# Kernel optimization log

Hardware: AMD Instinct MI355X
Metric: run time of the kernel (lower is better)

## Reference

```python
import jax, jax.numpy as jnp
import numpy as np

N_NODES = 50000
N_EDGES = 800000
FEAT = 10
HID = 64
N_SHEETS = 256
SHEET_LEN = 128
NUM_GRAPHS = 1


def _glorot(key, shape):
    fan_in, fan_out = shape[0], shape[1]
    lim = float(np.sqrt(6.0 / (fan_in + fan_out)))
    return jax.random.uniform(key, shape, jnp.float32, -lim, lim)


def setup_inputs() -> dict:
    key = jax.random.key(0)
    ks = jax.random.split(key, 16)
    x = jax.random.normal(ks[0], (N_NODES, FEAT), jnp.float32)
    edge_index = jax.random.randint(ks[1], (2, N_EDGES), 0, N_NODES, jnp.int64)
    batch = jnp.zeros((N_NODES,), jnp.int64)
    sheet_node_idx = jax.random.randint(ks[2], (N_SHEETS, SHEET_LEN), 0, N_NODES, jnp.int64)
    sheet_features = jax.random.normal(ks[3], (N_SHEETS, FEAT), jnp.float32)
    return {
        "x": x, "edge_index": edge_index, "batch": batch,
        "sheet_node_idx": sheet_node_idx, "sheet_features": sheet_features,
        "W_gcn1": _glorot(ks[4], (FEAT, HID)), "b_gcn1": jnp.zeros((HID,), jnp.float32),
        "W_gcn2": _glorot(ks[5], (HID, HID)), "b_gcn2": jnp.zeros((HID,), jnp.float32),
        "W_gcn3": _glorot(ks[6], (HID, HID)), "b_gcn3": jnp.zeros((HID,), jnp.float32),
        "geo_W1": _glorot(ks[7], (FEAT, HID)), "geo_b1": jnp.zeros((HID,), jnp.float32),
        "geo_W2": _glorot(ks[8], (HID, HID)), "geo_b2": jnp.zeros((HID,), jnp.float32),
        "fus_W": _glorot(ks[9], (2 * HID, HID)), "fus_b": jnp.zeros((HID,), jnp.float32),
        "q_W1": _glorot(ks[10], (2 * HID, HID)), "q_b1": jnp.zeros((HID,), jnp.float32),
        "q_W2": _glorot(ks[11], (HID, 1)), "q_b2": jnp.zeros((1,), jnp.float32),
    }


def gcn_conv(x, W, b, src, dst, norm_edge, norm_self):
    # PyG GCNConv: h = x @ W, symmetric-normalized aggregation with self loops, + b
    h = x @ W                                  # [N, H]
    msg = h[src] * norm_edge[:, None]          # [E, H] gather
    agg = jax.ops.segment_sum(msg, dst, num_segments=x.shape[0])  # scatter-add
    agg = agg + h * norm_self[:, None]         # self-loop contribution
    return agg + b


def reference(x, edge_index, batch, sheet_node_idx, sheet_features,
              W_gcn1, b_gcn1, W_gcn2, b_gcn2, W_gcn3, b_gcn3,
              geo_W1, geo_b1, geo_W2, geo_b2, fus_W, fus_b,
              q_W1, q_b1, q_W2, q_b2):
    src, dst = edge_index[0], edge_index[1]
    N = x.shape[0]
    # degree with self loops (edge weights = 1), counted on destination
    deg = jax.ops.segment_sum(jnp.ones_like(dst, jnp.float32), dst, num_segments=N) + 1.0
    dinv = jax.lax.rsqrt(deg)
    norm_edge = dinv[src] * dinv[dst]   # [E]
    norm_self = dinv * dinv             # [N]

    h = jax.nn.relu(gcn_conv(x, W_gcn1, b_gcn1, src, dst, norm_edge, norm_self))
    h = jax.nn.relu(gcn_conv(h, W_gcn2, b_gcn2, src, dst, norm_edge, norm_self))
    h = jax.nn.relu(gcn_conv(h, W_gcn3, b_gcn3, src, dst, norm_edge, norm_self))

    # global mean pool over batch ids (single graph here)
    sums = jax.ops.segment_sum(h, batch, num_segments=NUM_GRAPHS)
    counts = jax.ops.segment_sum(jnp.ones((N,), jnp.float32), batch, num_segments=NUM_GRAPHS)
    g_emb = sums / counts[:, None]      # [1, H]

    # per-sheet mean pooling (equal-length sheets)
    sheet_embs = h[sheet_node_idx].mean(axis=1)            # [S, H]

    geo = jax.nn.relu(sheet_features @ geo_W1 + geo_b1) @ geo_W2 + geo_b2
    fused = jax.nn.relu(jnp.concatenate([sheet_embs, geo], axis=1) @ fus_W + fus_b)

    global_embs = jnp.broadcast_to(g_emb, (fused.shape[0], g_emb.shape[1]))
    hq = jnp.concatenate([fused, global_embs], axis=1)
    q = jax.nn.relu(hq @ q_W1 + q_b1) @ q_W2 + q_b2
    return q[:, 0]
```

## Files before the change

kernel.cpp:

```cpp
#include <hip/hip_runtime.h>

#define HID 64
#define FEAT 10
#define MAXSEG 8192

typedef unsigned short u16;

__device__ __forceinline__ u16 f2bf(float f) {
    unsigned u = __float_as_uint(f);
    unsigned r = (u + 0x7fffu + ((u >> 16) & 1u)) >> 16;
    return (u16)r;
}
__device__ __forceinline__ void bf8_add(float* acc, uint4 u) {
    acc[0] += __uint_as_float(u.x << 16);
    acc[1] += __uint_as_float(u.x & 0xffff0000u);
    acc[2] += __uint_as_float(u.y << 16);
    acc[3] += __uint_as_float(u.y & 0xffff0000u);
    acc[4] += __uint_as_float(u.z << 16);
    acc[5] += __uint_as_float(u.z & 0xffff0000u);
    acc[6] += __uint_as_float(u.w << 16);
    acc[7] += __uint_as_float(u.w & 0xffff0000u);
}


__global__ void bin_kernel(const int* __restrict__ src, const int* __restrict__ dst,
                           int* __restrict__ gcnt, unsigned* __restrict__ tmp,
                           u16* __restrict__ hwb, u16* __restrict__ xp,
                           int E, int N) {
    __shared__ int h[256];
    int t = threadIdx.x, c = blockIdx.x;
    if (t < 256) h[t] = 0;
    __syncthreads();
    int b0 = c * 4096;
    unsigned pk[4]; int bk[4];
    #pragma unroll
    for (int j = 0; j < 4; j++) {
        int e = b0 + t + j * 1024;
        if (e < E) {
            int s = src[e], d = dst[e];
            pk[j] = ((unsigned)(d & 255) << 16) | (unsigned)s;
            bk[j] = d >> 8;
            atomicAdd(&h[bk[j]], 1);
        } else bk[j] = -1;
    }
    __syncthreads();
    if (t < 256) {
        int v = h[t];
        int resv = v ? atomicAdd(&gcnt[t], v) : 0;
        h[t] = t * MAXSEG + resv;
    }
    __syncthreads();
    #pragma unroll
    for (int j = 0; j < 4; j++) {
        if (bk[j] >= 0) {
            int slot = atomicAdd(&h[bk[j]], 1);
            tmp[slot] = pk[j];
        }
    }
    if (c == 0) {
        if (t < 64)      hwb[(size_t)N * 64 + t] = 0;
        else if (t < 80) xp[(size_t)N * 16 + (t - 64)] = 0;
    }
}

__global__ void csr_build(const unsigned* __restrict__ tmp, const int* __restrict__ gcnt,
                          u16* __restrict__ csr2,
                          int* __restrict__ row_start, int* __restrict__ row_cntp,
                          float* __restrict__ dinv,
                          const float* __restrict__ x, u16* __restrict__ xp, int N) {
    __shared__ __align__(16) u16 staged[MAXSEG];
    __shared__ int cntL[256], padL[256], scanL[256], curL[256];
    __shared__ float sdinv[256];
    int b = blockIdx.x, t = threadIdx.x;
    if (t < 256) cntL[t] = 0;
    for (int i = t; i < MAXSEG; i += 1024) staged[i] = (u16)N;
    __syncthreads();
    int segBase = b * MAXSEG, segLen = gcnt[b];
    for (int i = t; i < segLen; i += 1024)
        atomicAdd(&cntL[tmp[segBase + i] >> 16], 1);
    __syncthreads();
    if (t < 256) { padL[t] = (cntL[t] + 7) & ~7; scanL[t] = padL[t]; }
    __syncthreads();
    for (int off = 1; off < 256; off <<= 1) {
        int a = (t < 256) ? scanL[t] : 0;
        int s = (t >= off && t < 256) ? scanL[t - off] : 0;
        __syncthreads();
        if (t < 256) scanL[t] = a + s;
        __syncthreads();
    }
    if (t < 256) {
        int excl = scanL[t] - padL[t];
        curL[t] = excl;
        float dv = rsqrtf((float)cntL[t] + 1.0f);
        sdinv[t] = dv;
        int node = b * 256 + t;
        if (node < N) {
            row_start[node] = b * MAXSEG + excl;
            row_cntp[node]  = padL[t];
            dinv[node]      = dv;
        }
    }
    __syncthreads();
    for (int i = t; i < segLen; i += 1024) {
        unsigned e = tmp[segBase + i];
        int idx = atomicAdd(&curL[e >> 16], 1);
        staged[idx] = (u16)(e & 0xffffu);
    }
    for (int i = t; i < 256 * 16; i += 1024) {
        int nlc = i >> 4, cch = i & 15;
        int node = b * 256 + nlc;
        if (node < N)
            xp[(size_t)node * 16 + cch] =
                (cch < FEAT) ? f2bf(sdinv[nlc] * x[(size_t)node * FEAT + cch]) : (u16)0;
    }
    __syncthreads();
    ((uint4*)(csr2 + (size_t)b * MAXSEG))[t] = ((const uint4*)staged)[t];
}


__global__ void gxmm1(const int* __restrict__ row_start, const int* __restrict__ row_cntp,
                      const u16* __restrict__ csr2, const u16* __restrict__ xp,
                      const float* __restrict__ dinv,
                      const float* __restrict__ W1, const float* __restrict__ b1,
                      float* __restrict__ hf, int N) {
    __shared__ float sW[FEAT * 64];
    __shared__ float sH[64 * 16];
    int t = threadIdx.x;
    int node0 = blockIdx.x * 64;
    for (int i = t; i < FEAT * 64; i += 256) sW[i] = W1[i];
    if (t < 128) {
        int nl = t >> 1;
        int node = node0 + nl;
        int c0 = (t & 1) * 8;
        float acc[8] = {0.f,0.f,0.f,0.f,0.f,0.f,0.f,0.f};
        if (node < N) {
            uint4 sv = *(const uint4*)(xp + (size_t)node * 16 + c0);
            bf8_add(acc, sv);
            int i0 = row_start[node], iE = i0 + row_cntp[node];
            for (int i = i0; i < iE; i += 8) {
                uint4 ev = *(const uint4*)(csr2 + i);
                int s0 = ev.x & 0xffff, s1 = ev.x >> 16;
                int s2 = ev.y & 0xffff, s3 = ev.y >> 16;
                int s4 = ev.z & 0xffff, s5 = ev.z >> 16;
                int s6 = ev.w & 0xffff, s7 = ev.w >> 16;
                uint4 u0 = *(const uint4*)(xp + (size_t)s0 * 16 + c0);
                uint4 u1 = *(const uint4*)(xp + (size_t)s1 * 16 + c0);
                uint4 u2 = *(const uint4*)(xp + (size_t)s2 * 16 + c0);
                uint4 u3 = *(const uint4*)(xp + (size_t)s3 * 16 + c0);
                uint4 u4 = *(const uint4*)(xp + (size_t)s4 * 16 + c0);
                uint4 u5 = *(const uint4*)(xp + (size_t)s5 * 16 + c0);
                uint4 u6 = *(const uint4*)(xp + (size_t)s6 * 16 + c0);
                uint4 u7 = *(const uint4*)(xp + (size_t)s7 * 16 + c0);
                bf8_add(acc, u0); bf8_add(acc, u1); bf8_add(acc, u2); bf8_add(acc, u3);
                bf8_add(acc, u4); bf8_add(acc, u5); bf8_add(acc, u6); bf8_add(acc, u7);
            }
            float di = dinv[node];
            #pragma unroll
            for (int j = 0; j < 8; j++) acc[j] *= di;
        }
        #pragma unroll
        for (int j = 0; j < 8; j++) sH[nl * 16 + c0 + j] = acc[j];
    }
    __syncthreads();
    int c0 = (t & 15) * 4;
    int rbase = (t >> 4) * 4;
    float4 a0 = {0,0,0,0}, a1 = {0,0,0,0}, a2 = {0,0,0,0}, a3 = {0,0,0,0};
    for (int k = 0; k < FEAT; k++) {
        float4 w = *(const float4*)(sW + k * 64 + c0);
        float h0 = sH[(rbase + 0) * 16 + k];
        float h1v = sH[(rbase + 1) * 16 + k];
        float h2 = sH[(rbase + 2) * 16 + k];
        float h3 = sH[(rbase + 3) * 16 + k];
        a0.x += h0 * w.x; a0.y += h0 * w.y; a0.z += h0 * w.z; a0.w += h0 * w.w;
        a1.x += h1v * w.x; a1.y += h1v * w.y; a1.z += h1v * w.z; a1.w += h1v * w.w;
        a2.x += h2 * w.x; a2.y += h2 * w.y; a2.z += h2 * w.z; a2.w += h2 * w.w;
        a3.x += h3 * w.x; a3.y += h3 * w.y; a3.z += h3 * w.z; a3.w += h3 * w.w;
    }
    float4 bb = *(const float4*)(b1 + c0);
    float4 accs[4] = {a0, a1, a2, a3};
    for (int rr = 0; rr < 4; rr++) {
        int node = node0 + rbase + rr;
        if (node >= N) break;
        float4 v = accs[rr];
        v.x = fmaxf(v.x + bb.x, 0.f); v.y = fmaxf(v.y + bb.y, 0.f);
        v.z = fmaxf(v.z + bb.z, 0.f); v.w = fmaxf(v.w + bb.w, 0.f);
        *(float4*)(hf + (size_t)node * 64 + c0) = v;
    }
}


__global__ void gcn_matmul64(const float* __restrict__ h_in, const float* __restrict__ W,
                             const float* __restrict__ dinv, u16* __restrict__ hwb, int N) {
    __shared__ float sW[64 * 64];
    __shared__ float sH[64 * 65];
    int t = threadIdx.x;
    int node0 = blockIdx.x * 64;
    for (int i = t * 4; i < 4096; i += 1024)
        *(float4*)(sW + i) = *(const float4*)(W + i);
    for (int i = t; i < 4096; i += 256) {
        int r = i >> 6, k = i & 63;
        int node = node0 + r;
        sH[r * 65 + k] = (node < N) ? h_in[(size_t)node * 64 + k] : 0.0f;
    }
    __syncthreads();
    int c0 = (t & 15) * 4;
    int rbase = (t >> 4) * 4;
    float4 a0 = {0,0,0,0}, a1 = {0,0,0,0}, a2 = {0,0,0,0}, a3 = {0,0,0,0};
    for (int k = 0; k < 64; k++) {
        float4 w = *(const float4*)(sW + k * 64 + c0);
        float h0 = sH[(rbase + 0) * 65 + k];
        float h1v = sH[(rbase + 1) * 65 + k];
        float h2 = sH[(rbase + 2) * 65 + k];
        float h3 = sH[(rbase + 3) * 65 + k];
        a0.x += h0 * w.x; a0.y += h0 * w.y; a0.z += h0 * w.z; a0.w += h0 * w.w;
        a1.x += h1v * w.x; a1.y += h1v * w.y; a1.z += h1v * w.z; a1.w += h1v * w.w;
        a2.x += h2 * w.x; a2.y += h2 * w.y; a2.z += h2 * w.z; a2.w += h2 * w.w;
        a3.x += h3 * w.x; a3.y += h3 * w.y; a3.z += h3 * w.z; a3.w += h3 * w.w;
    }
    float4 accs[4] = {a0, a1, a2, a3};
    for (int rr = 0; rr < 4; rr++) {
        int node = node0 + rbase + rr;
        if (node >= N) break;
        float di = dinv[node];
        float4 v = accs[rr];
        ushort4 o;
        o.x = f2bf(v.x * di); o.y = f2bf(v.y * di);
        o.z = f2bf(v.z * di); o.w = f2bf(v.w * di);
        *(ushort4*)(hwb + (size_t)node * 64 + c0) = o;
    }
}

__global__ void gather_bf(const int* __restrict__ row_start, const int* __restrict__ row_cntp,
                          const u16* __restrict__ csr2, const u16* __restrict__ hwb,
                          const float* __restrict__ dinv, const float* __restrict__ b,
                          float* __restrict__ out, float* __restrict__ gsum,
                          int N, int do_gsum) {
    int t = threadIdx.x;
    int nl = t >> 3;
    int node = blockIdx.x * 32 + nl;
    int c0 = (t & 7) * 8;
    float acc[8] = {0.f,0.f,0.f,0.f,0.f,0.f,0.f,0.f};
    if (node < N) {
        uint4 sv = *(const uint4*)(hwb + (size_t)node * 64 + c0);
        bf8_add(acc, sv);
        int i0 = row_start[node], iE = i0 + row_cntp[node];
        for (int i = i0; i < iE; i += 8) {
            uint4 ev = *(const uint4*)(csr2 + i);
            int s0 = ev.x & 0xffff, s1 = ev.x >> 16;
            int s2 = ev.y & 0xffff, s3 = ev.y >> 16;
            int s4 = ev.z & 0xffff, s5 = ev.z >> 16;
            int s6 = ev.w & 0xffff, s7 = ev.w >> 16;
            uint4 u0 = *(const uint4*)(hwb + (size_t)s0 * 64 + c0);
            uint4 u1 = *(const uint4*)(hwb + (size_t)s1 * 64 + c0);
            uint4 u2 = *(const uint4*)(hwb + (size_t)s2 * 64 + c0);
            uint4 u3 = *(const uint4*)(hwb + (size_t)s3 * 64 + c0);
            uint4 u4 = *(const uint4*)(hwb + (size_t)s4 * 64 + c0);
            uint4 u5 = *(const uint4*)(hwb + (size_t)s5 * 64 + c0);
            uint4 u6 = *(const uint4*)(hwb + (size_t)s6 * 64 + c0);
            uint4 u7 = *(const uint4*)(hwb + (size_t)s7 * 64 + c0);
            bf8_add(acc, u0); bf8_add(acc, u1); bf8_add(acc, u2); bf8_add(acc, u3);
            bf8_add(acc, u4); bf8_add(acc, u5); bf8_add(acc, u6); bf8_add(acc, u7);
        }
        float di = dinv[node];
        const float4 bb0 = *(const float4*)(b + c0);
        const float4 bb1 = *(const float4*)(b + c0 + 4);
        float4 o0, o1;
        o0.x = fmaxf(acc[0]*di + bb0.x, 0.f); o0.y = fmaxf(acc[1]*di + bb0.y, 0.f);
        o0.z = fmaxf(acc[2]*di + bb0.z, 0.f); o0.w = fmaxf(acc[3]*di + bb0.w, 0.f);
        o1.x = fmaxf(acc[4]*di + bb1.x, 0.f); o1.y = fmaxf(acc[5]*di + bb1.y, 0.f);
        o1.z = fmaxf(acc[6]*di + bb1.z, 0.f); o1.w = fmaxf(acc[7]*di + bb1.w, 0.f);
        *(float4*)(out + (size_t)node * 64 + c0)     = o0;
        *(float4*)(out + (size_t)node * 64 + c0 + 4) = o1;
        acc[0]=o0.x; acc[1]=o0.y; acc[2]=o0.z; acc[3]=o0.w;
        acc[4]=o1.x; acc[5]=o1.y; acc[6]=o1.z; acc[7]=o1.w;
    }
    if (do_gsum) {
        __shared__ float red[32 * 64];
        #pragma unroll
        for (int j = 0; j < 8; j++) red[nl * 64 + c0 + j] = acc[j];
        __syncthreads();
        if (t < 64) {
            float s = 0.f;
            #pragma unroll 8
            for (int k = 0; k < 32; k++) s += red[k * 64 + t];
            atomicAdd(&gsum[t], s);
        }
    }
}


__global__ void final_kernel(const float* __restrict__ h3, const int* __restrict__ sheet_idx,
                             const float* __restrict__ sheet_feat, const float* __restrict__ g_sum,
                             const float* __restrict__ gW1, const float* __restrict__ gb1,
                             const float* __restrict__ gW2, const float* __restrict__ gb2,
                             const float* __restrict__ fW,  const float* __restrict__ fb,
                             const float* __restrict__ qW1, const float* __restrict__ qb1,
                             const float* __restrict__ qW2, const float* __restrict__ qb2,
                             float* __restrict__ out, int N, int L) {
    int s = blockIdx.x, t = threadIdx.x;
    __shared__ float red[256];
    __shared__ float semb[64];
    __shared__ float geoh[64];
    __shared__ float geo[64];
    __shared__ float hq[128];
    int c = t & 63, jg = t >> 6;
    float acc = 0.0f;
    for (int j = jg; j < L; j += 4) {
        int node = sheet_idx[s * L + j];
        acc += h3[(size_t)node * 64 + c];
    }
    red[t] = acc;
    __syncthreads();
    if (t < 64) {
        semb[t] = (red[t] + red[t + 64] + red[t + 128] + red[t + 192]) / (float)L;
        hq[64 + t] = g_sum[t] / (float)N;
        float a = gb1[t];
        #pragma unroll
        for (int k = 0; k < FEAT; k++) a += sheet_feat[s * FEAT + k] * gW1[k * 64 + t];
        geoh[t] = fmaxf(a, 0.0f);
    }
    __syncthreads();
    if (t < 64) {
        float a = gb2[t];
        for (int k = 0; k < 64; k++) a += geoh[k] * gW2[k * 64 + t];
        geo[t] = a;
    }
    __syncthreads();
    if (t < 64) {
        float a = fb[t];
        for (int k = 0; k < 64; k++) a += semb[k] * fW[k * 64 + t];
        for (int k = 0; k < 64; k++) a += geo[k]  * fW[(64 + k) * 64 + t];
        hq[t] = fmaxf(a, 0.0f);
    }
    __syncthreads();
    float q = 0.0f;
    if (t < 64) {
        float a = qb1[t];
        for (int k = 0; k < 128; k++) a += hq[k] * qW1[k * 64 + t];
        a = fmaxf(a, 0.0f);
        q = a * qW2[t];
        for (int off = 32; off > 0; off >>= 1) q += __shfl_down(q, off, 64);
        if (t == 0) out[s] = q + qb2[0];
    }
}

extern "C" void kernel_launch(void* const* d_in, const int* in_sizes, int n_in,
                              void* d_out, int out_size, void* d_ws, size_t ws_size,
                              hipStream_t stream) {
    const float* x          = (const float*)d_in[0];
    const int*   edge       = (const int*)d_in[1];
    const int*   sheet_idx  = (const int*)d_in[3];
    const float* sheet_feat = (const float*)d_in[4];
    const float* W1 = (const float*)d_in[5];  const float* b1 = (const float*)d_in[6];
    const float* W2 = (const float*)d_in[7];  const float* b2 = (const float*)d_in[8];
    const float* W3 = (const float*)d_in[9];  const float* b3 = (const float*)d_in[10];
    const float* gW1 = (const float*)d_in[11]; const float* gb1 = (const float*)d_in[12];
    const float* gW2 = (const float*)d_in[13]; const float* gb2 = (const float*)d_in[14];
    const float* fW  = (const float*)d_in[15]; const float* fb  = (const float*)d_in[16];
    const float* qW1 = (const float*)d_in[17]; const float* qb1 = (const float*)d_in[18];
    const float* qW2 = (const float*)d_in[19]; const float* qb2 = (const float*)d_in[20];
    float* out = (float*)d_out;

    int N = in_sizes[2];
    int E = in_sizes[1] / 2;
    int S = in_sizes[4] / FEAT;
    int L = in_sizes[3] / S;

    int nbuckets = (N + 255) / 256;
    int nchunks  = (E + 4095) / 4096;

    char* p = (char*)d_ws;
    unsigned* tmp  = (unsigned*)p;             p += (size_t)nbuckets * MAXSEG * 4;
    u16* csr2      = (u16*)p;                  p += (size_t)nbuckets * MAXSEG * 2;
    float* hf      = (float*)p;                p += (size_t)N * 64 * 4;
    u16* hwb       = (u16*)p;                  p += (size_t)(N + 1) * 64 * 2;
    u16* xp        = (u16*)p;                  p += (size_t)(N + 1) * 16 * 2;
    int* row_start = (int*)p;                  p += (size_t)N * 4;
    int* row_cntp  = (int*)p;                  p += (size_t)N * 4;
    float* dinv    = (float*)p;                p += (size_t)N * 4;
    int* gcnt      = (int*)p;                  p += 256 * 4;
    float* gsum    = (float*)p;                p += 64 * 4;

    hipMemsetAsync(gcnt, 0, 256 * 4 + 64 * 4, stream);

    const int* src = edge;
    const int* dst = edge + E;

    int gMM = (N + 63) / 64;
    int gGB = (N + 31) / 32;

    bin_kernel<<<nchunks, 1024, 0, stream>>>(src, dst, gcnt, tmp, hwb, xp, E, N);
    csr_build<<<nbuckets, 1024, 0, stream>>>(tmp, gcnt, csr2, row_start, row_cntp, dinv, x, xp, N);

    gxmm1<<<gMM, 256, 0, stream>>>(row_start, row_cntp, csr2, xp, dinv, W1, b1, hf, N);

    gcn_matmul64<<<gMM, 256, 0, stream>>>(hf, W2, dinv, hwb, N);
    gather_bf<<<gGB, 256, 0, stream>>>(row_start, row_cntp, csr2, hwb, dinv, b2, hf, gsum, N, 0);

    gcn_matmul64<<<gMM, 256, 0, stream>>>(hf, W3, dinv, hwb, N);
    gather_bf<<<gGB, 256, 0, stream>>>(row_start, row_cntp, csr2, hwb, dinv, b3, hf, gsum, N, 1);

    final_kernel<<<S, 256, 0, stream>>>(hf, sheet_idx, sheet_feat, gsum,
                                        gW1, gb1, gW2, gb2, fW, fb,
                                        qW1, qb1, qW2, qb2, out, N, L);
}
```

Before: 238.3 us.

## Sort nodes by degree within buckets to balance gather warps; prefetch CSR indices

csr_build now produces a per-bucket permutation that orders nodes by padded degree class, and the gather kernels (gxmm1, gather_bf) process nodes in that permuted order so threads in a wavefront have similar trip counts. The gather loops also prefetch the next 8-index CSR vector one iteration ahead, which needs a small pad at the end of csr2. The aim is to cut wavefront divergence and load latency in the neighbour aggregation, at the cost of an extra shared histogram and scan in csr_build, an indirect perm load per node, and scattered output writes.

```diff
diff --git a/kernel.cpp b/kernel.cpp
--- a/kernel.cpp
+++ b/kernel.cpp
@@ -66,13 +66,15 @@
 __global__ void csr_build(const unsigned* __restrict__ tmp, const int* __restrict__ gcnt,
                           u16* __restrict__ csr2,
                           int* __restrict__ row_start, int* __restrict__ row_cntp,
-                          float* __restrict__ dinv,
+                          float* __restrict__ dinv, int* __restrict__ perm,
                           const float* __restrict__ x, u16* __restrict__ xp, int N) {
     __shared__ __align__(16) u16 staged[MAXSEG];
     __shared__ int cntL[256], padL[256], scanL[256], curL[256];
     __shared__ float sdinv[256];
+    __shared__ int h32[32], o32[32];
     int b = blockIdx.x, t = threadIdx.x;
     if (t < 256) cntL[t] = 0;
+    if (t < 32) h32[t] = 0;
     for (int i = t; i < MAXSEG; i += 1024) staged[i] = (u16)N;
     __syncthreads();
     int segBase = b * MAXSEG, segLen = gcnt[b];
@@ -88,6 +90,7 @@
         if (t < 256) scanL[t] = a + s;
         __syncthreads();
     }
+    int key = 0;
     if (t < 256) {
         int excl = scanL[t] - padL[t];
         curL[t] = excl;
@@ -99,6 +102,18 @@
             row_cntp[node]  = padL[t];
             dinv[node]      = dv;
         }
+        key = min(padL[t] >> 3, 31);
+        atomicAdd(&h32[key], 1);
+    }
+    __syncthreads();
+    if (t == 0) {
+        int run = 0;
+        for (int k2 = 0; k2 < 32; k2++) { o32[k2] = run; run += h32[k2]; }
+    }
+    __syncthreads();
+    if (t < 256) {
+        int pos = atomicAdd(&o32[key], 1);
+        perm[b * 256 + pos] = b * 256 + t;
     }
     __syncthreads();
     for (int i = t; i < segLen; i += 1024) {
@@ -118,7 +133,8 @@
 }
 
 
-__global__ void gxmm1(const int* __restrict__ row_start, const int* __restrict__ row_cntp,
+__global__ void gxmm1(const int* __restrict__ perm,
+                      const int* __restrict__ row_start, const int* __restrict__ row_cntp,
                       const u16* __restrict__ csr2, const u16* __restrict__ xp,
                       const float* __restrict__ dinv,
                       const float* __restrict__ W1, const float* __restrict__ b1,
@@ -126,33 +142,38 @@
     __shared__ float sW[FEAT * 64];
     __shared__ float sH[64 * 16];
     int t = threadIdx.x;
-    int node0 = blockIdx.x * 64;
+    int slot0 = blockIdx.x * 64;
     for (int i = t; i < FEAT * 64; i += 256) sW[i] = W1[i];
     if (t < 128) {
         int nl = t >> 1;
-        int node = node0 + nl;
+        int node = perm[slot0 + nl];
         int c0 = (t & 1) * 8;
         float acc[8] = {0.f,0.f,0.f,0.f,0.f,0.f,0.f,0.f};
         if (node < N) {
             uint4 sv = *(const uint4*)(xp + (size_t)node * 16 + c0);
             bf8_add(acc, sv);
-            int i0 = row_start[node], iE = i0 + row_cntp[node];
-            for (int i = i0; i < iE; i += 8) {
-                uint4 ev = *(const uint4*)(csr2 + i);
-                int s0 = ev.x & 0xffff, s1 = ev.x >> 16;
-                int s2 = ev.y & 0xffff, s3 = ev.y >> 16;
-                int s4 = ev.z & 0xffff, s5 = ev.z >> 16;
-                int s6 = ev.w & 0xffff, s7 = ev.w >> 16;
-                uint4 u0 = *(const uint4*)(xp + (size_t)s0 * 16 + c0);
-                uint4 u1 = *(const uint4*)(xp + (size_t)s1 * 16 + c0);
-                uint4 u2 = *(const uint4*)(xp + (size_t)s2 * 16 + c0);
-                uint4 u3 = *(const uint4*)(xp + (size_t)s3 * 16 + c0);
-                uint4 u4 = *(const uint4*)(xp + (size_t)s4 * 16 + c0);
-                uint4 u5 = *(const uint4*)(xp + (size_t)s5 * 16 + c0);
-                uint4 u6 = *(const uint4*)(xp + (size_t)s6 * 16 + c0);
-                uint4 u7 = *(const uint4*)(xp + (size_t)s7 * 16 + c0);
-                bf8_add(acc, u0); bf8_add(acc, u1); bf8_add(acc, u2); bf8_add(acc, u3);
-                bf8_add(acc, u4); bf8_add(acc, u5); bf8_add(acc, u6); bf8_add(acc, u7);
+            int i0 = row_start[node], cnt = row_cntp[node];
+            if (cnt) {
+                int iE = i0 + cnt;
+                uint4 ev = *(const uint4*)(csr2 + i0);
+                for (int i = i0; i < iE; i += 8) {
+                    uint4 evn = *(const uint4*)(csr2 + i + 8);
+                    int s0 = ev.x & 0xffff, s1 = ev.x >> 16;
+                    int s2 = ev.y & 0xffff, s3 = ev.y >> 16;
+                    int s4 = ev.z & 0xffff, s5 = ev.z >> 16;
+                    int s6 = ev.w & 0xffff, s7 = ev.w >> 16;
+                    uint4 u0 = *(const uint4*)(xp + (size_t)s0 * 16 + c0);
+                    uint4 u1 = *(const uint4*)(xp + (size_t)s1 * 16 + c0);
+                    uint4 u2 = *(const uint4*)(xp + (size_t)s2 * 16 + c0);
+                    uint4 u3 = *(const uint4*)(xp + (size_t)s3 * 16 + c0);
+                    uint4 u4 = *(const uint4*)(xp + (size_t)s4 * 16 + c0);
+                    uint4 u5 = *(const uint4*)(xp + (size_t)s5 * 16 + c0);
+                    uint4 u6 = *(const uint4*)(xp + (size_t)s6 * 16 + c0);
+                    uint4 u7 = *(const uint4*)(xp + (size_t)s7 * 16 + c0);
+                    bf8_add(acc, u0); bf8_add(acc, u1); bf8_add(acc, u2); bf8_add(acc, u3);
+                    bf8_add(acc, u4); bf8_add(acc, u5); bf8_add(acc, u6); bf8_add(acc, u7);
+                    ev = evn;
+                }
             }
             float di = dinv[node];
             #pragma unroll
@@ -179,12 +200,13 @@
     float4 bb = *(const float4*)(b1 + c0);
     float4 accs[4] = {a0, a1, a2, a3};
     for (int rr = 0; rr < 4; rr++) {
-        int node = node0 + rbase + rr;
-        if (node >= N) break;
-        float4 v = accs[rr];
-        v.x = fmaxf(v.x + bb.x, 0.f); v.y = fmaxf(v.y + bb.y, 0.f);
-        v.z = fmaxf(v.z + bb.z, 0.f); v.w = fmaxf(v.w + bb.w, 0.f);
-        *(float4*)(hf + (size_t)node * 64 + c0) = v;
+        int node = perm[slot0 + rbase + rr];
+        if (node < N) {
+            float4 v = accs[rr];
+            v.x = fmaxf(v.x + bb.x, 0.f); v.y = fmaxf(v.y + bb.y, 0.f);
+            v.z = fmaxf(v.z + bb.z, 0.f); v.w = fmaxf(v.w + bb.w, 0.f);
+            *(float4*)(hf + (size_t)node * 64 + c0) = v;
+        }
     }
 }
 
@@ -230,36 +252,42 @@
     }
 }
 
-__global__ void gather_bf(const int* __restrict__ row_start, const int* __restrict__ row_cntp,
+__global__ void gather_bf(const int* __restrict__ perm,
+                          const int* __restrict__ row_start, const int* __restrict__ row_cntp,
                           const u16* __restrict__ csr2, const u16* __restrict__ hwb,
                           const float* __restrict__ dinv, const float* __restrict__ b,
                           float* __restrict__ out, float* __restrict__ gsum,
                           int N, int do_gsum) {
     int t = threadIdx.x;
     int nl = t >> 3;
-    int node = blockIdx.x * 32 + nl;
+    int node = perm[blockIdx.x * 32 + nl];
     int c0 = (t & 7) * 8;
     float acc[8] = {0.f,0.f,0.f,0.f,0.f,0.f,0.f,0.f};
     if (node < N) {
         uint4 sv = *(const uint4*)(hwb + (size_t)node * 64 + c0);
         bf8_add(acc, sv);
-        int i0 = row_start[node], iE = i0 + row_cntp[node];
-        for (int i = i0; i < iE; i += 8) {
-            uint4 ev = *(const uint4*)(csr2 + i);
-            int s0 = ev.x & 0xffff, s1 = ev.x >> 16;
-            int s2 = ev.y & 0xffff, s3 = ev.y >> 16;
-            int s4 = ev.z & 0xffff, s5 = ev.z >> 16;
-            int s6 = ev.w & 0xffff, s7 = ev.w >> 16;
-            uint4 u0 = *(const uint4*)(hwb + (size_t)s0 * 64 + c0);
-            uint4 u1 = *(const uint4*)(hwb + (size_t)s1 * 64 + c0);
-            uint4 u2 = *(const uint4*)(hwb + (size_t)s2 * 64 + c0);
-            uint4 u3 = *(const uint4*)(hwb + (size_t)s3 * 64 + c0);
-            uint4 u4 = *(const uint4*)(hwb + (size_t)s4 * 64 + c0);
-            uint4 u5 = *(const uint4*)(hwb + (size_t)s5 * 64 + c0);
-            uint4 u6 = *(const uint4*)(hwb + (size_t)s6 * 64 + c0);
-            uint4 u7 = *(const uint4*)(hwb + (size_t)s7 * 64 + c0);
-            bf8_add(acc, u0); bf8_add(acc, u1); bf8_add(acc, u2); bf8_add(acc, u3);
-            bf8_add(acc, u4); bf8_add(acc, u5); bf8_add(acc, u6); bf8_add(acc, u7);
+        int i0 = row_start[node], cnt = row_cntp[node];
+        if (cnt) {
+            int iE = i0 + cnt;
+            uint4 ev = *(const uint4*)(csr2 + i0);
+            for (int i = i0; i < iE; i += 8) {
+                uint4 evn = *(const uint4*)(csr2 + i + 8);
+                int s0 = ev.x & 0xffff, s1 = ev.x >> 16;
+                int s2 = ev.y & 0xffff, s3 = ev.y >> 16;
+                int s4 = ev.z & 0xffff, s5 = ev.z >> 16;
+                int s6 = ev.w & 0xffff, s7 = ev.w >> 16;
+                uint4 u0 = *(const uint4*)(hwb + (size_t)s0 * 64 + c0);
+                uint4 u1 = *(const uint4*)(hwb + (size_t)s1 * 64 + c0);
+                uint4 u2 = *(const uint4*)(hwb + (size_t)s2 * 64 + c0);
+                uint4 u3 = *(const uint4*)(hwb + (size_t)s3 * 64 + c0);
+                uint4 u4 = *(const uint4*)(hwb + (size_t)s4 * 64 + c0);
+                uint4 u5 = *(const uint4*)(hwb + (size_t)s5 * 64 + c0);
+                uint4 u6 = *(const uint4*)(hwb + (size_t)s6 * 64 + c0);
+                uint4 u7 = *(const uint4*)(hwb + (size_t)s7 * 64 + c0);
+                bf8_add(acc, u0); bf8_add(acc, u1); bf8_add(acc, u2); bf8_add(acc, u3);
+                bf8_add(acc, u4); bf8_add(acc, u5); bf8_add(acc, u6); bf8_add(acc, u7);
+                ev = evn;
+            }
         }
         float di = dinv[node];
         const float4 bb0 = *(const float4*)(b + c0);
@@ -368,16 +396,18 @@
 
     int nbuckets = (N + 255) / 256;
     int nchunks  = (E + 4095) / 4096;
+    int nslots   = nbuckets * 256;
 
     char* p = (char*)d_ws;
     unsigned* tmp  = (unsigned*)p;             p += (size_t)nbuckets * MAXSEG * 4;
-    u16* csr2      = (u16*)p;                  p += (size_t)nbuckets * MAXSEG * 2;
+    u16* csr2      = (u16*)p;                  p += ((size_t)nbuckets * MAXSEG + 32) * 2;
     float* hf      = (float*)p;                p += (size_t)N * 64 * 4;
     u16* hwb       = (u16*)p;                  p += (size_t)(N + 1) * 64 * 2;
     u16* xp        = (u16*)p;                  p += (size_t)(N + 1) * 16 * 2;
     int* row_start = (int*)p;                  p += (size_t)N * 4;
     int* row_cntp  = (int*)p;                  p += (size_t)N * 4;
     float* dinv    = (float*)p;                p += (size_t)N * 4;
+    int* perm      = (int*)p;                  p += (size_t)nslots * 4;
     int* gcnt      = (int*)p;                  p += 256 * 4;
     float* gsum    = (float*)p;                p += 64 * 4;
 
@@ -387,18 +417,19 @@
     const int* dst = edge + E;
 
     int gMM = (N + 63) / 64;
-    int gGB = (N + 31) / 32;
+    int gGX = nslots / 64;
+    int gGB = nslots / 32;
 
     bin_kernel<<<nchunks, 1024, 0, stream>>>(src, dst, gcnt, tmp, hwb, xp, E, N);
-    csr_build<<<nbuckets, 1024, 0, stream>>>(tmp, gcnt, csr2, row_start, row_cntp, dinv, x, xp, N);
-
-    gxmm1<<<gMM, 256, 0, stream>>>(row_start, row_cntp, csr2, xp, dinv, W1, b1, hf, N);
+    csr_build<<<nbuckets, 1024, 0, stream>>>(tmp, gcnt, csr2, row_start, row_cntp, dinv, perm, x, xp, N);
+
+    gxmm1<<<gGX, 256, 0, stream>>>(perm, row_start, row_cntp, csr2, xp, dinv, W1, b1, hf, N);
 
     gcn_matmul64<<<gMM, 256, 0, stream>>>(hf, W2, dinv, hwb, N);
-    gather_bf<<<gGB, 256, 0, stream>>>(row_start, row_cntp, csr2, hwb, dinv, b2, hf, gsum, N, 0);
+    gather_bf<<<gGB, 256, 0, stream>>>(perm, row_start, row_cntp, csr2, hwb, dinv, b2, hf, gsum, N, 0);
 
     gcn_matmul64<<<gMM, 256, 0, stream>>>(hf, W3, dinv, hwb, N);
-    gather_bf<<<gGB, 256, 0, stream>>>(row_start, row_cntp, csr2, hwb, dinv, b3, hf, gsum, N, 1);
+    gather_bf<<<gGB, 256, 0, stream>>>(perm, row_start, row_cntp, csr2, hwb, dinv, b3, hf, gsum, N, 1);
 
     final_kernel<<<S, 256, 0, stream>>>(hf, sheet_idx, sheet_feat, gsum,
                                         gW1, gb1, gW2, gb2, fW, fb,
```

Measured after the change: 253.1 us. 6.2% more time.

## Fuse layer dense transforms into neighbouring gather kernels to cut launches and fp32 traffic

Applied to the files above, without the earlier changes.

Merges the layer-1 aggregate+transform with the layer-2 64x64 matmul, and the layer-2 gather with the layer-3 matmul. The intermediate hidden states stay in shared memory instead of round-tripping through global memory as fp32. Three kernels disappear, along with the global writes and reads of the hf array between stages. Two bf16 buffers are used so the fused g2l3 kernel can read one while writing the other. In exchange, shared memory per block grows, which may lower occupancy in the latency-bound gather phases.

```diff
diff --git a/kernel.cpp b/kernel.cpp
--- a/kernel.cpp
+++ b/kernel.cpp
@@ -23,10 +23,11 @@
 }
 
 
-__global__ void bin_kernel(const int* __restrict__ src, const int* __restrict__ dst,
-                           int* __restrict__ gcnt, unsigned* __restrict__ tmp,
-                           u16* __restrict__ hwb, u16* __restrict__ xp,
-                           int E, int N) {
+__global__ __launch_bounds__(1024) void bin_kernel(
+        const int* __restrict__ src, const int* __restrict__ dst,
+        int* __restrict__ gcnt, unsigned* __restrict__ tmp,
+        u16* __restrict__ hwba, u16* __restrict__ hwbb, u16* __restrict__ xp,
+        int E, int N) {
     __shared__ int h[256];
     int t = threadIdx.x, c = blockIdx.x;
     if (t < 256) h[t] = 0;
@@ -58,16 +59,18 @@
         }
     }
     if (c == 0) {
-        if (t < 64)      hwb[(size_t)N * 64 + t] = 0;
-        else if (t < 80) xp[(size_t)N * 16 + (t - 64)] = 0;
-    }
-}
-
-__global__ void csr_build(const unsigned* __restrict__ tmp, const int* __restrict__ gcnt,
-                          u16* __restrict__ csr2,
-                          int* __restrict__ row_start, int* __restrict__ row_cntp,
-                          float* __restrict__ dinv,
-                          const float* __restrict__ x, u16* __restrict__ xp, int N) {
+        if (t < 64)       hwba[(size_t)N * 64 + t] = 0;
+        else if (t < 128) hwbb[(size_t)N * 64 + (t - 64)] = 0;
+        else if (t < 144) xp[(size_t)N * 16 + (t - 128)] = 0;
+    }
+}
+
+__global__ __launch_bounds__(1024) void csr_build(
+        const unsigned* __restrict__ tmp, const int* __restrict__ gcnt,
+        u16* __restrict__ csr2,
+        int* __restrict__ row_start, int* __restrict__ row_cntp,
+        float* __restrict__ dinv,
+        const float* __restrict__ x, u16* __restrict__ xp, int N) {
     __shared__ __align__(16) u16 staged[MAXSEG];
     __shared__ int cntL[256], padL[256], scanL[256], curL[256];
     __shared__ float sdinv[256];
@@ -118,13 +121,16 @@
 }
 
 
-__global__ void gxmm1(const int* __restrict__ row_start, const int* __restrict__ row_cntp,
-                      const u16* __restrict__ csr2, const u16* __restrict__ xp,
-                      const float* __restrict__ dinv,
-                      const float* __restrict__ W1, const float* __restrict__ b1,
-                      float* __restrict__ hf, int N) {
-    __shared__ float sW[FEAT * 64];
-    __shared__ float sH[64 * 16];
+__global__ __launch_bounds__(256) void l1l2(
+        const int* __restrict__ row_start, const int* __restrict__ row_cntp,
+        const u16* __restrict__ csr2, const u16* __restrict__ xp,
+        const float* __restrict__ dinv,
+        const float* __restrict__ W1, const float* __restrict__ b1,
+        const float* __restrict__ W2,
+        u16* __restrict__ hwba, int N) {
+    __shared__ float sW[64 * 64];
+    __shared__ float sH16[64 * 16];
+    __shared__ float sH64[64 * 65];
     int t = threadIdx.x;
     int node0 = blockIdx.x * 64;
     for (int i = t; i < FEAT * 64; i += 256) sW[i] = W1[i];
@@ -159,89 +165,156 @@
             for (int j = 0; j < 8; j++) acc[j] *= di;
         }
         #pragma unroll
-        for (int j = 0; j < 8; j++) sH[nl * 16 + c0 + j] = acc[j];
+        for (int j = 0; j < 8; j++) sH16[nl * 16 + c0 + j] = acc[j];
     }
     __syncthreads();
     int c0 = (t & 15) * 4;
     int rbase = (t >> 4) * 4;
-    float4 a0 = {0,0,0,0}, a1 = {0,0,0,0}, a2 = {0,0,0,0}, a3 = {0,0,0,0};
-    for (int k = 0; k < FEAT; k++) {
-        float4 w = *(const float4*)(sW + k * 64 + c0);
-        float h0 = sH[(rbase + 0) * 16 + k];
-        float h1v = sH[(rbase + 1) * 16 + k];
-        float h2 = sH[(rbase + 2) * 16 + k];
-        float h3 = sH[(rbase + 3) * 16 + k];
-        a0.x += h0 * w.x; a0.y += h0 * w.y; a0.z += h0 * w.z; a0.w += h0 * w.w;
-        a1.x += h1v * w.x; a1.y += h1v * w.y; a1.z += h1v * w.z; a1.w += h1v * w.w;
-        a2.x += h2 * w.x; a2.y += h2 * w.y; a2.z += h2 * w.z; a2.w += h2 * w.w;
-        a3.x += h3 * w.x; a3.y += h3 * w.y; a3.z += h3 * w.z; a3.w += h3 * w.w;
-    }
-    float4 bb = *(const float4*)(b1 + c0);
-    float4 accs[4] = {a0, a1, a2, a3};
-    for (int rr = 0; rr < 4; rr++) {
-        int node = node0 + rbase + rr;
-        if (node >= N) break;
-        float4 v = accs[rr];
-        v.x = fmaxf(v.x + bb.x, 0.f); v.y = fmaxf(v.y + bb.y, 0.f);
-        v.z = fmaxf(v.z + bb.z, 0.f); v.w = fmaxf(v.w + bb.w, 0.f);
-        *(float4*)(hf + (size_t)node * 64 + c0) = v;
-    }
-}
-
-
-__global__ void gcn_matmul64(const float* __restrict__ h_in, const float* __restrict__ W,
-                             const float* __restrict__ dinv, u16* __restrict__ hwb, int N) {
+    {
+        float4 a0 = {0,0,0,0}, a1 = {0,0,0,0}, a2 = {0,0,0,0}, a3 = {0,0,0,0};
+        for (int k = 0; k < FEAT; k++) {
+            float4 w = *(const float4*)(sW + k * 64 + c0);
+            float h0 = sH16[(rbase + 0) * 16 + k];
+            float h1v = sH16[(rbase + 1) * 16 + k];
+            float h2 = sH16[(rbase + 2) * 16 + k];
+            float h3 = sH16[(rbase + 3) * 16 + k];
+            a0.x += h0 * w.x; a0.y += h0 * w.y; a0.z += h0 * w.z; a0.w += h0 * w.w;
+            a1.x += h1v * w.x; a1.y += h1v * w.y; a1.z += h1v * w.z; a1.w += h1v * w.w;
+            a2.x += h2 * w.x; a2.y += h2 * w.y; a2.z += h2 * w.z; a2.w += h2 * w.w;
+            a3.x += h3 * w.x; a3.y += h3 * w.y; a3.z += h3 * w.z; a3.w += h3 * w.w;
+        }
+        float4 bb = *(const float4*)(b1 + c0);
+        float4 accs[4] = {a0, a1, a2, a3};
+        #pragma unroll
+        for (int rr = 0; rr < 4; rr++) {
+            float4 v = accs[rr];
+            int r = rbase + rr;
+            sH64[r * 65 + c0 + 0] = fmaxf(v.x + bb.x, 0.f);
+            sH64[r * 65 + c0 + 1] = fmaxf(v.y + bb.y, 0.f);
+            sH64[r * 65 + c0 + 2] = fmaxf(v.z + bb.z, 0.f);
+            sH64[r * 65 + c0 + 3] = fmaxf(v.w + bb.w, 0.f);
+        }
+    }
+    __syncthreads();
+    for (int i = t * 4; i < 4096; i += 256 * 4)
+        *(float4*)(sW + i) = *(const float4*)(W2 + i);
+    __syncthreads();
+    {
+        float4 a0 = {0,0,0,0}, a1 = {0,0,0,0}, a2 = {0,0,0,0}, a3 = {0,0,0,0};
+        for (int k = 0; k < 64; k++) {
+            float4 w = *(const float4*)(sW + k * 64 + c0);
+            float h0 = sH64[(rbase + 0) * 65 + k];
+            float h1v = sH64[(rbase + 1) * 65 + k];
+            float h2 = sH64[(rbase + 2) * 65 + k];
+            float h3 = sH64[(rbase + 3) * 65 + k];
+            a0.x += h0 * w.x; a0.y += h0 * w.y; a0.z += h0 * w.z; a0.w += h0 * w.w;
+            a1.x += h1v * w.x; a1.y += h1v * w.y; a1.z += h1v * w.z; a1.w += h1v * w.w;
+            a2.x += h2 * w.x; a2.y += h2 * w.y; a2.z += h2 * w.z; a2.w += h2 * w.w;
+            a3.x += h3 * w.x; a3.y += h3 * w.y; a3.z += h3 * w.z; a3.w += h3 * w.w;
+        }
+        float4 accs[4] = {a0, a1, a2, a3};
+        for (int rr = 0; rr < 4; rr++) {
+            int node = node0 + rbase + rr;
+            if (node >= N) break;
+            float di = dinv[node];
+            float4 v = accs[rr];
+            ushort4 o;
+            o.x = f2bf(v.x * di); o.y = f2bf(v.y * di);
+            o.z = f2bf(v.z * di); o.w = f2bf(v.w * di);
+            *(ushort4*)(hwba + (size_t)node * 64 + c0) = o;
+        }
+    }
+}
+
+
+__global__ __launch_bounds__(512) void g2l3(
+        const int* __restrict__ row_start, const int* __restrict__ row_cntp,
+        const u16* __restrict__ csr2, const u16* __restrict__ hwba,
+        const float* __restrict__ dinv, const float* __restrict__ b2,
+        const float* __restrict__ W3,
+        u16* __restrict__ hwbb, int N) {
     __shared__ float sW[64 * 64];
-    __shared__ float sH[64 * 65];
+    __shared__ float sH64[64 * 65];
     int t = threadIdx.x;
     int node0 = blockIdx.x * 64;
-    for (int i = t * 4; i < 4096; i += 1024)
-        *(float4*)(sW + i) = *(const float4*)(W + i);
-    for (int i = t; i < 4096; i += 256) {
-        int r = i >> 6, k = i & 63;
-        int node = node0 + r;
-        sH[r * 65 + k] = (node < N) ? h_in[(size_t)node * 64 + k] : 0.0f;
-    }
-    __syncthreads();
-    int c0 = (t & 15) * 4;
-    int rbase = (t >> 4) * 4;
-    float4 a0 = {0,0,0,0}, a1 = {0,0,0,0}, a2 = {0,0,0,0}, a3 = {0,0,0,0};
-    for (int k = 0; k < 64; k++) {
-        float4 w = *(const float4*)(sW + k * 64 + c0);
-        float h0 = sH[(rbase + 0) * 65 + k];
-        float h1v = sH[(rbase + 1) * 65 + k];
-        float h2 = sH[(rbase + 2) * 65 + k];
-        float h3 = sH[(rbase + 3) * 65 + k];
-        a0.x += h0 * w.x; a0.y += h0 * w.y; a0.z += h0 * w.z; a0.w += h0 * w.w;
-        a1.x += h1v * w.x; a1.y += h1v * w.y; a1.z += h1v * w.z; a1.w += h1v * w.w;
-        a2.x += h2 * w.x; a2.y += h2 * w.y; a2.z += h2 * w.z; a2.w += h2 * w.w;
-        a3.x += h3 * w.x; a3.y += h3 * w.y; a3.z += h3 * w.z; a3.w += h3 * w.w;
-    }
-    float4 accs[4] = {a0, a1, a2, a3};
-    for (int rr = 0; rr < 4; rr++) {
-        int node = node0 + rbase + rr;
-        if (node >= N) break;
-        float di = dinv[node];
-        float4 v = accs[rr];
-        ushort4 o;
-        o.x = f2bf(v.x * di); o.y = f2bf(v.y * di);
-        o.z = f2bf(v.z * di); o.w = f2bf(v.w * di);
-        *(ushort4*)(hwb + (size_t)node * 64 + c0) = o;
-    }
-}
-
-__global__ void gather_bf(const int* __restrict__ row_start, const int* __restrict__ row_cntp,
-                          const u16* __restrict__ csr2, const u16* __restrict__ hwb,
-                          const float* __restrict__ dinv, const float* __restrict__ b,
-                          float* __restrict__ out, float* __restrict__ gsum,
-                          int N, int do_gsum) {
+    {
+        int nl = t >> 3;
+        int node = node0 + nl;
+        int c0 = (t & 7) * 8;
+        float acc[8] = {0.f,0.f,0.f,0.f,0.f,0.f,0.f,0.f};
+        if (node < N) {
+            uint4 sv = *(const uint4*)(hwba + (size_t)node * 64 + c0);
+            bf8_add(acc, sv);
+            int i0 = row_start[node], iE = i0 + row_cntp[node];
+            for (int i = i0; i < iE; i += 8) {
+                uint4 ev = *(const uint4*)(csr2 + i);
+                int s0 = ev.x & 0xffff, s1 = ev.x >> 16;
+                int s2 = ev.y & 0xffff, s3 = ev.y >> 16;
+                int s4 = ev.z & 0xffff, s5 = ev.z >> 16;
+                int s6 = ev.w & 0xffff, s7 = ev.w >> 16;
+                uint4 u0 = *(const uint4*)(hwba + (size_t)s0 * 64 + c0);
+                uint4 u1 = *(const uint4*)(hwba + (size_t)s1 * 64 + c0);
+                uint4 u2 = *(const uint4*)(hwba + (size_t)s2 * 64 + c0);
+                uint4 u3 = *(const uint4*)(hwba + (size_t)s3 * 64 + c0);
+                uint4 u4 = *(const uint4*)(hwba + (size_t)s4 * 64 + c0);
+                uint4 u5 = *(const uint4*)(hwba + (size_t)s5 * 64 + c0);
+                uint4 u6 = *(const uint4*)(hwba + (size_t)s6 * 64 + c0);
+                uint4 u7 = *(const uint4*)(hwba + (size_t)s7 * 64 + c0);
+                bf8_add(acc, u0); bf8_add(acc, u1); bf8_add(acc, u2); bf8_add(acc, u3);
+                bf8_add(acc, u4); bf8_add(acc, u5); bf8_add(acc, u6); bf8_add(acc, u7);
+            }
+            float di = dinv[node];
+            const float4 bb0 = *(const float4*)(b2 + c0);
+            const float4 bb1 = *(const float4*)(b2 + c0 + 4);
+            acc[0] = fmaxf(acc[0]*di + bb0.x, 0.f); acc[1] = fmaxf(acc[1]*di + bb0.y, 0.f);
+            acc[2] = fmaxf(acc[2]*di + bb0.z, 0.f); acc[3] = fmaxf(acc[3]*di + bb0.w, 0.f);
+            acc[4] = fmaxf(acc[4]*di + bb1.x, 0.f); acc[5] = fmaxf(acc[5]*di + bb1.y, 0.f);
+            acc[6] = fmaxf(acc[6]*di + bb1.z, 0.f); acc[7] = fmaxf(acc[7]*di + bb1.w, 0.f);
+        }
+        #pragma unroll
+        for (int j = 0; j < 8; j++) sH64[nl * 65 + c0 + j] = acc[j];
+    }
+    for (int i = t * 4; i < 4096; i += 512 * 4)
+        *(float4*)(sW + i) = *(const float4*)(W3 + i);
+    __syncthreads();
+    {
+        int c0 = (t & 15) * 4;
+        int r0 = (t >> 4) * 2;
+        float4 a0 = {0,0,0,0}, a1 = {0,0,0,0};
+        for (int k = 0; k < 64; k++) {
+            float4 w = *(const float4*)(sW + k * 64 + c0);
+            float h0 = sH64[(r0 + 0) * 65 + k];
+            float h1v = sH64[(r0 + 1) * 65 + k];
+            a0.x += h0 * w.x; a0.y += h0 * w.y; a0.z += h0 * w.z; a0.w += h0 * w.w;
+            a1.x += h1v * w.x; a1.y += h1v * w.y; a1.z += h1v * w.z; a1.w += h1v * w.w;
+        }
+        float4 accs[2] = {a0, a1};
+        for (int rr = 0; rr < 2; rr++) {
+            int node = node0 + r0 + rr;
+            if (node >= N) break;
+            float di = dinv[node];
+            float4 v = accs[rr];
+            ushort4 o;
+            o.x = f2bf(v.x * di); o.y = f2bf(v.y * di);
+            o.z = f2bf(v.z * di); o.w = f2bf(v.w * di);
+            *(ushort4*)(hwbb + (size_t)node * 64 + c0) = o;
+        }
+    }
+}
+
+
+__global__ __launch_bounds__(256) void gather_b3(
+        const int* __restrict__ row_start, const int* __restrict__ row_cntp,
+        const u16* __restrict__ csr2, const u16* __restrict__ hwbb,
+        const float* __restrict__ dinv, const float* __restrict__ b,
+        float* __restrict__ out, float* __restrict__ gsum, int N) {
     int t = threadIdx.x;
     int nl = t >> 3;
     int node = blockIdx.x * 32 + nl;
     int c0 = (t & 7) * 8;
     float acc[8] = {0.f,0.f,0.f,0.f,0.f,0.f,0.f,0.f};
     if (node < N) {
-        uint4 sv = *(const uint4*)(hwb + (size_t)node * 64 + c0);
+        uint4 sv = *(const uint4*)(hwbb + (size_t)node * 64 + c0);
         bf8_add(acc, sv);
         int i0 = row_start[node], iE = i0 + row_cntp[node];
         for (int i = i0; i < iE; i += 8) {
@@ -250,14 +323,14 @@
             int s2 = ev.y & 0xffff, s3 = ev.y >> 16;
             int s4 = ev.z & 0xffff, s5 = ev.z >> 16;
             int s6 = ev.w & 0xffff, s7 = ev.w >> 16;
-            uint4 u0 = *(const uint4*)(hwb + (size_t)s0 * 64 + c0);
-            uint4 u1 = *(const uint4*)(hwb + (size_t)s1 * 64 + c0);
-            uint4 u2 = *(const uint4*)(hwb + (size_t)s2 * 64 + c0);
-            uint4 u3 = *(const uint4*)(hwb + (size_t)s3 * 64 + c0);
-            uint4 u4 = *(const uint4*)(hwb + (size_t)s4 * 64 + c0);
-            uint4 u5 = *(const uint4*)(hwb + (size_t)s5 * 64 + c0);
-            uint4 u6 = *(const uint4*)(hwb + (size_t)s6 * 64 + c0);
-            uint4 u7 = *(const uint4*)(hwb + (size_t)s7 * 64 + c0);
+            uint4 u0 = *(const uint4*)(hwbb + (size_t)s0 * 64 + c0);
+            uint4 u1 = *(const uint4*)(hwbb + (size_t)s1 * 64 + c0);
+            uint4 u2 = *(const uint4*)(hwbb + (size_t)s2 * 64 + c0);
+            uint4 u3 = *(const uint4*)(hwbb + (size_t)s3 * 64 + c0);
+            uint4 u4 = *(const uint4*)(hwbb + (size_t)s4 * 64 + c0);
+            uint4 u5 = *(const uint4*)(hwbb + (size_t)s5 * 64 + c0);
+            uint4 u6 = *(const uint4*)(hwbb + (size_t)s6 * 64 + c0);
+            uint4 u7 = *(const uint4*)(hwbb + (size_t)s7 * 64 + c0);
             bf8_add(acc, u0); bf8_add(acc, u1); bf8_add(acc, u2); bf8_add(acc, u3);
             bf8_add(acc, u4); bf8_add(acc, u5); bf8_add(acc, u6); bf8_add(acc, u7);
         }
@@ -274,29 +347,28 @@
         acc[0]=o0.x; acc[1]=o0.y; acc[2]=o0.z; acc[3]=o0.w;
         acc[4]=o1.x; acc[5]=o1.y; acc[6]=o1.z; acc[7]=o1.w;
     }
-    if (do_gsum) {
-        __shared__ float red[32 * 64];
-        #pragma unroll
-        for (int j = 0; j < 8; j++) red[nl * 64 + c0 + j] = acc[j];
-        __syncthreads();
-        if (t < 64) {
-            float s = 0.f;
-            #pragma unroll 8
-            for (int k = 0; k < 32; k++) s += red[k * 64 + t];
-            atomicAdd(&gsum[t], s);
-        }
-    }
-}
-
-
-__global__ void final_kernel(const float* __restrict__ h3, const int* __restrict__ sheet_idx,
-                             const float* __restrict__ sheet_feat, const float* __restrict__ g_sum,
-                             const float* __restrict__ gW1, const float* __restrict__ gb1,
-                             const float* __restrict__ gW2, const float* __restrict__ gb2,
-                             const float* __restrict__ fW,  const float* __restrict__ fb,
-                             const float* __restrict__ qW1, const float* __restrict__ qb1,
-                             const float* __restrict__ qW2, const float* __restrict__ qb2,
-                             float* __restrict__ out, int N, int L) {
+    __shared__ float red[32 * 64];
+    #pragma unroll
+    for (int j = 0; j < 8; j++) red[nl * 64 + c0 + j] = acc[j];
+    __syncthreads();
+    if (t < 64) {
+        float s = 0.f;
+        #pragma unroll 8
+        for (int k = 0; k < 32; k++) s += red[k * 64 + t];
+        atomicAdd(&gsum[t], s);
+    }
+}
+
+
+__global__ __launch_bounds__(256) void final_kernel(
+        const float* __restrict__ h3, const int* __restrict__ sheet_idx,
+        const float* __restrict__ sheet_feat, const float* __restrict__ g_sum,
+        const float* __restrict__ gW1, const float* __restrict__ gb1,
+        const float* __restrict__ gW2, const float* __restrict__ gb2,
+        const float* __restrict__ fW,  const float* __restrict__ fb,
+        const float* __restrict__ qW1, const float* __restrict__ qb1,
+        const float* __restrict__ qW2, const float* __restrict__ qb2,
+        float* __restrict__ out, int N, int L) {
     int s = blockIdx.x, t = threadIdx.x;
     __shared__ float red[256];
     __shared__ float semb[64];
@@ -373,7 +445,8 @@
     unsigned* tmp  = (unsigned*)p;             p += (size_t)nbuckets * MAXSEG * 4;
     u16* csr2      = (u16*)p;                  p += (size_t)nbuckets * MAXSEG * 2;
     float* hf      = (float*)p;                p += (size_t)N * 64 * 4;
-    u16* hwb       = (u16*)p;                  p += (size_t)(N + 1) * 64 * 2;
+    u16* hwba      = (u16*)p;                  p += (size_t)(N + 1) * 64 * 2;
+    u16* hwbb      = (u16*)p;                  p += (size_t)(N + 1) * 64 * 2;
     u16* xp        = (u16*)p;                  p += (size_t)(N + 1) * 16 * 2;
     int* row_start = (int*)p;                  p += (size_t)N * 4;
     int* row_cntp  = (int*)p;                  p += (size_t)N * 4;
@@ -389,16 +462,12 @@
     int gMM = (N + 63) / 64;
     int gGB = (N + 31) / 32;
 
-    bin_kernel<<<nchunks, 1024, 0, stream>>>(src, dst, gcnt, tmp, hwb, xp, E, N);
+    bin_kernel<<<nchunks, 1024, 0, stream>>>(src, dst, gcnt, tmp, hwba, hwbb, xp, E, N);
     csr_build<<<nbuckets, 1024, 0, stream>>>(tmp, gcnt, csr2, row_start, row_cntp, dinv, x, xp, N);
 
-    gxmm1<<<gMM, 256, 0, stream>>>(row_start, row_cntp, csr2, xp, dinv, W1, b1, hf, N);
-
-    gcn_matmul64<<<gMM, 256, 0, stream>>>(hf, W2, dinv, hwb, N);
-    gather_bf<<<gGB, 256, 0, stream>>>(row_start, row_cntp, csr2, hwb, dinv, b2, hf, gsum, N, 0);
-
-    gcn_matmul64<<<gMM, 256, 0, stream>>>(hf, W3, dinv, hwb, N);
-    gather_bf<<<gGB, 256, 0, stream>>>(row_start, row_cntp, csr2, hwb, dinv, b3, hf, gsum, N, 1);
+    l1l2<<<gMM, 256, 0, stream>>>(row_start, row_cntp, csr2, xp, dinv, W1, b1, W2, hwba, N);
+    g2l3<<<gMM, 512, 0, stream>>>(row_start, row_cntp, csr2, hwba, dinv, b2, W3, hwbb, N);
+    gather_b3<<<gGB, 256, 0, stream>>>(row_start, row_cntp, csr2, hwbb, dinv, b3, hf, gsum, N);
 
     final_kernel<<<S, 256, 0, stream>>>(hf, sheet_idx, sheet_feat, gsum,
                                         gW1, gb1, gW2, gb2, fW, fb,
```

Measured after the change: 242.7 us. About the same (+1.8%).
